# Performance work log

Hardware: AMD Instinct MI355X
Metric: run time of the kernel (lower is better)

Reference implementation:

```python
import jax, jax.numpy as jnp
import numpy as np

B, S, R, C_M = 1, 512, 256, 256   # batch, n_seq, n_res, msa channels
C_P, C_Z = 32, 128                # projection channels, pair channels


def setup_inputs() -> dict:
    key = jax.random.key(0)
    ks = jax.random.split(key, 8)
    M = jax.random.normal(ks[0], (B, S, R, C_M), dtype=jnp.float32)
    M_mask = jnp.ones((B, S, R), dtype=jnp.float32)
    Z_raw = jnp.zeros((B, R, R, C_Z), dtype=jnp.float32)
    # LayerNorm params
    ln_g = jnp.ones((C_M,), dtype=jnp.float32)
    ln_b = jnp.zeros((C_M,), dtype=jnp.float32)
    # linear_a / linear_b: glorot-uniform init
    lim = float(np.sqrt(6.0 / (C_M + C_P)))
    Wa = jax.random.uniform(ks[1], (C_P, C_M), minval=-lim, maxval=lim, dtype=jnp.float32)
    ba = jnp.zeros((C_P,), dtype=jnp.float32)
    Wb = jax.random.uniform(ks[2], (C_P, C_M), minval=-lim, maxval=lim, dtype=jnp.float32)
    bb = jnp.zeros((C_P,), dtype=jnp.float32)
    # o_linear is zero-initialized in the source; use small random weights so the
    # output is non-trivial for correctness testing (math is identical).
    Wo = jax.random.normal(ks[3], (C_Z, C_P * C_P), dtype=jnp.float32) * 0.02
    bo = jnp.zeros((C_Z,), dtype=jnp.float32)
    return {"M": M, "M_mask": M_mask, "Z_raw": Z_raw, "ln_g": ln_g, "ln_b": ln_b,
            "Wa": Wa, "ba": ba, "Wb": Wb, "bb": bb, "Wo": Wo, "bo": bo}


def _layernorm(x, g, b, eps=1e-5):
    mu = jnp.mean(x, axis=-1, keepdims=True)
    var = jnp.var(x, axis=-1, keepdims=True)
    return (x - mu) * jax.lax.rsqrt(var + eps) * g + b


def reference(M, M_mask, Z_raw, ln_g, ln_b, Wa, ba, Wb, bb, Wo, bo):
    Mn = _layernorm(M, ln_g, ln_b)                      # [b,s,i,c_m]
    mask = M_mask[..., None]                            # [b,s,i,1]
    left = (jnp.einsum('bsic,dc->bsid', Mn, Wa) + ba) * mask   # [b,s,i,d]
    right = (jnp.einsum('bsic,ec->bsie', Mn, Wb) + bb) * mask  # [b,s,j,e]
    # outer-product mean: contract over sequence dim s
    O = jnp.einsum('bsid,bsje->bijde', left, right)     # [b,i,j,d,e]
    b, i, j, d, e = O.shape
    O = O.reshape(b, i, j, d * e)
    Z = jnp.einsum('bijk,zk->bijz', O, Wo) + bo         # [b,i,j,c_z]
    norm = jnp.einsum('bsi,bsj->bij', M_mask, M_mask)[..., None]
    return Z / (1e-3 + norm)
```

## Files before the change

kernel.cpp:

```cpp
#include <hip/hip_runtime.h>
#include <hip/hip_bf16.h>
#include <stdint.h>

#define S_DIM 512
#define R_DIM 256
#define CM 256
#define CP 32
#define CZ 128

typedef __attribute__((ext_vector_type(8))) short bf16x8;
typedef __attribute__((ext_vector_type(4))) float f32x4;
typedef __attribute__((ext_vector_type(16))) float f32x16;
typedef unsigned int u32;

__device__ __forceinline__ float bf2f(unsigned short u) {
  union { u32 i; float f; } v; v.i = ((u32)u) << 16; return v.f;
}
__device__ __forceinline__ unsigned short f2bf(float f) {
  union { float f; u32 i; } v; v.f = f;
  u32 x = v.i;
  u32 r = (x + 0x7FFFu + ((x >> 16) & 1u)) >> 16;
  return (unsigned short)r;
}

__device__ __forceinline__ void gload_lds16(const unsigned short* g, unsigned short* l) {
  __builtin_amdgcn_global_load_lds((const __attribute__((address_space(1))) u32*)(g),
                                   (__attribute__((address_space(3))) u32*)(l), 16, 0, 0);
}

__device__ __forceinline__ void wave_bar() {
  asm volatile("" ::: "memory");
  __builtin_amdgcn_s_barrier();
  asm volatile("" ::: "memory");
}

__global__ __launch_bounds__(256) void
fused_prep_kernel(const float* __restrict__ Wa, const float* __restrict__ ba,
                  const float* __restrict__ Wb, const float* __restrict__ bb,
                  const float* __restrict__ ln_g, const float* __restrict__ ln_b,
                  const float* __restrict__ Wo, const float* __restrict__ mask,
                  unsigned short* __restrict__ wp, float* __restrict__ Ka,
                  float* __restrict__ Ca, unsigned short* __restrict__ Wo_bf,
                  float* __restrict__ scale) {
  const int b = blockIdx.x;
  const int t = threadIdx.x;
  if (b < 64) {
    __shared__ float ska[4], sca[4];
    const int o = b;
    const float* W = (o < 32) ? (Wa + o * CM) : (Wb + (o - 32) * CM);
    float wv = W[t];
    unsigned short bv = f2bf(wv * ln_g[t]);
    wp[o * CM + t] = bv;
    float ka = bf2f(bv);
    float ca = wv * ln_b[t];
    #pragma unroll
    for (int m = 1; m < 64; m <<= 1) {
      ka += __shfl_xor(ka, m);
      ca += __shfl_xor(ca, m);
    }
    if ((t & 63) == 0) { ska[t >> 6] = ka; sca[t >> 6] = ca; }
    __syncthreads();
    if (t == 0) {
      Ka[o] = ska[0] + ska[1] + ska[2] + ska[3];
      Ca[o] = sca[0] + sca[1] + sca[2] + sca[3] + ((o < 32) ? ba[o] : bb[o - 32]);
    }
  } else if (b < 576) {
    int idx = (b - 64) * 256 + t;
    int z = idx >> 10, k = idx & 1023;
    int d = k >> 5, e = k & 31;
    Wo_bf[(z << 10) + e * 32 + d] = f2bf(Wo[idx]);
  } else {
    const int i = b - 576, j = t;
    float sum = 0.f;
    for (int s = 0; s < S_DIM; ++s)
      sum += mask[s * R_DIM + i] * mask[s * R_DIM + j];
    scale[i * R_DIM + j] = 1.0f / (1e-3f + sum);
  }
}

#define K1_ROWS 64
#define XPAD 264

__global__ __launch_bounds__(256) void
ln_proj_kernel(const float* __restrict__ M, const float* __restrict__ mask,
               const unsigned short* __restrict__ wp_g, const float* __restrict__ Ka_g,
               const float* __restrict__ Ca_g,
               unsigned short* __restrict__ leftT, unsigned short* __restrict__ rightT) {
  __shared__ unsigned short xt[K1_ROWS * XPAD];
  __shared__ unsigned short wp[64 * XPAD];
  __shared__ float smu[K1_ROWS], srs[K1_ROWS], smk[K1_ROWS];
  __shared__ float sKa[64], sCa[64];

  const int t = threadIdx.x;
  const int lane = t & 63;
  const int w = t >> 6;
  const int lm = lane & 15;
  const int rr = lane >> 4;
  const int i = blockIdx.x;
  const int s0 = blockIdx.y * K1_ROWS;

  for (int idx = t; idx < 64 * CM / 8; idx += 256) {
    int row = idx >> 5;
    int col = (idx & 31) * 8;
    *(uint4*)(&wp[row * XPAD + col]) = *(const uint4*)(wp_g + row * CM + col);
  }
  if (t < 64) { sKa[t] = Ka_g[t]; sCa[t] = Ca_g[t]; }

  #pragma unroll
  for (int it = 0; it < 4; ++it) {
    const int row = w * 16 + it * 4 + rr;
    const int sg = s0 + row;
    const float* src = M + ((size_t)sg * R_DIM + i) * CM;
    float4 x[4];
    #pragma unroll
    for (int ch = 0; ch < 4; ++ch) x[ch] = *(const float4*)(src + ch * 64 + lm * 4);
    float sum = 0.f, ssq = 0.f;
    #pragma unroll
    for (int ch = 0; ch < 4; ++ch) {
      sum += x[ch].x + x[ch].y + x[ch].z + x[ch].w;
      ssq += x[ch].x * x[ch].x + x[ch].y * x[ch].y + x[ch].z * x[ch].z + x[ch].w * x[ch].w;
    }
    #pragma unroll
    for (int m = 1; m < 16; m <<= 1) {
      sum += __shfl_xor(sum, m);
      ssq += __shfl_xor(ssq, m);
    }
    float mu = sum * (1.0f / CM);
    float var = ssq * (1.0f / CM) - mu * mu;
    float rs = rsqrtf(var + 1e-5f);
    if (lm == 0) {
      smu[row] = mu; srs[row] = rs;
      smk[row] = mask[(size_t)sg * R_DIM + i];
    }
    #pragma unroll
    for (int ch = 0; ch < 4; ++ch) {
      ushort4 xb;
      xb.x = f2bf(x[ch].x); xb.y = f2bf(x[ch].y); xb.z = f2bf(x[ch].z); xb.w = f2bf(x[ch].w);
      *(ushort4*)(&xt[row * XPAD + ch * 64 + lm * 4]) = xb;
    }
  }
  __syncthreads();

  f32x4 acc[4] = {{0.f, 0.f, 0.f, 0.f}, {0.f, 0.f, 0.f, 0.f},
                  {0.f, 0.f, 0.f, 0.f}, {0.f, 0.f, 0.f, 0.f}};
  #pragma unroll
  for (int k = 0; k < 8; ++k) {
    const int c0 = k * 32 + ((lane >> 4) << 3);
    bf16x8 a = *(const bf16x8*)(&wp[(w * 16 + (lane & 15)) * XPAD + c0]);
    #pragma unroll
    for (int nt = 0; nt < 4; ++nt) {
      bf16x8 b = *(const bf16x8*)(&xt[(nt * 16 + (lane & 15)) * XPAD + c0]);
      acc[nt] = __builtin_amdgcn_mfma_f32_16x16x32_bf16(a, b, acc[nt], 0, 0, 0);
    }
  }

  #pragma unroll
  for (int nt = 0; nt < 4; ++nt) {
    int srow = nt * 16 + (lane & 15);
    float mu = smu[srow], rs = srs[srow], mk = smk[srow];
    int sg = s0 + srow;
    const size_t base = (size_t)(sg >> 3) * 65536 + (sg & 7);
    #pragma unroll
    for (int r = 0; r < 4; ++r) {
      int o = w * 16 + ((lane >> 4) << 2) + r;
      float v = (rs * (acc[nt][r] - mu * sKa[o]) + sCa[o]) * mk;
      unsigned short bv = f2bf(v);
      if (o < 32) leftT[base + (size_t)(i * 32 + o) * 8] = bv;
      else        rightT[base + (size_t)(i * 32 + (o - 32)) * 8] = bv;
    }
  }
}

#define NT2 8

__global__ __launch_bounds__(512, 1) void
opm_gemm_kernel(const unsigned short* __restrict__ leftT, const unsigned short* __restrict__ rightT,
                const unsigned short* __restrict__ Wo_bf, const float* __restrict__ bo,
                const float* __restrict__ scale, float* __restrict__ out) {
  extern __shared__ unsigned short smem[];

  const int t = threadIdx.x;
  const int lane = t & 63;
  const int l31 = lane & 31, lq2 = lane >> 5;
  const int w = t >> 6;
  const int wm = w >> 2, wn = w & 3;

  const int bid = blockIdx.x;
  const int xcd = bid & 7, local = bid >> 3;
  const int by = xcd * 4 + (local & 3);
  const int bx = local >> 2;

  const unsigned short* Asrc = leftT + (size_t)(by * 256) * 8;
  const unsigned short* Bsrc = rightT + (size_t)(bx * 256) * 8;

  int aoff[4], ldso[4];
  #pragma unroll
  for (int q = 0; q < 4; ++q) {
    int c = q * 512 + t;
    aoff[q] = (c >> 8) * 65536 + (c & 255) * 8;
    ldso[q] = c * 8;
  }

  f32x16 acc[4][2];
  #pragma unroll
  for (int a = 0; a < 4; ++a)
    #pragma unroll
    for (int b = 0; b < 2; ++b)
      #pragma unroll
      for (int r = 0; r < 16; ++r) acc[a][b][r] = 0.f;

  auto STAGE = [&](int kt, int buf) {
    const size_t kb = (size_t)kt * 8 * 65536;
    unsigned short* ab = smem + buf * 32768;
    #pragma unroll
    for (int q = 0; q < 4; ++q) {
      gload_lds16(Asrc + kb + aoff[q], ab + ldso[q]);
      gload_lds16(Bsrc + kb + aoff[q], ab + 16384 + ldso[q]);
    }
  };

  STAGE(0, 0);
  STAGE(1, 1);

  int arow[4], brow[2];
  #pragma unroll
  for (int mi = 0; mi < 4; ++mi) arow[mi] = (wm * 128 + mi * 32 + l31) * 8;
  #pragma unroll
  for (int ni = 0; ni < 2; ++ni) brow[ni] = 16384 + (wn * 64 + ni * 32 + l31) * 8;

  for (int kt = 0; kt < NT2; ++kt) {
    if (kt < NT2 - 1) asm volatile("s_waitcnt vmcnt(8)" ::: "memory");
    else              asm volatile("s_waitcnt vmcnt(0)" ::: "memory");
    wave_bar();

    const unsigned short* Ab = smem + (kt & 1) * 32768;
    #pragma unroll
    for (int ks = 0; ks < 4; ++ks) {
      const int kbase = (ks * 2 + lq2) * 2048;
      bf16x8 af[4], bf[2];
      #pragma unroll
      for (int mi = 0; mi < 4; ++mi) af[mi] = *(const bf16x8*)(Ab + kbase + arow[mi]);
      #pragma unroll
      for (int ni = 0; ni < 2; ++ni) bf[ni] = *(const bf16x8*)(Ab + kbase + brow[ni]);
      #pragma unroll
      for (int mi = 0; mi < 4; ++mi)
        #pragma unroll
        for (int ni = 0; ni < 2; ++ni)
          acc[mi][ni] = __builtin_amdgcn_mfma_f32_32x32x16_bf16(af[mi], bf[ni], acc[mi][ni], 0, 0, 0);
    }

    wave_bar();
    if (kt + 2 < NT2) STAGE(kt + 2, kt & 1);
  }

  #pragma unroll
  for (int mi = 0; mi < 4; ++mi) {
    #pragma unroll
    for (int ni = 0; ni < 2; ++ni) {
      const int pair = (wm * 4 + mi) * 8 + wn * 2 + ni;
      const u32 pbyte = (u32)((pair ^ l31) * 16 + lq2 * 8);
      #pragma unroll
      for (int g = 0; g < 4; ++g) {
        const u32 byte = (u32)(l31 * 4 + g) * 1024 + pbyte;
        ushort4 v4;
        v4.x = f2bf(acc[mi][ni][g * 4 + 0]);
        v4.y = f2bf(acc[mi][ni][g * 4 + 1]);
        v4.z = f2bf(acc[mi][ni][g * 4 + 2]);
        v4.w = f2bf(acc[mi][ni][g * 4 + 3]);
        *(ushort4*)((char*)smem + byte) = v4;
      }
    }
  }
  __syncthreads();

  f32x16 zacc;
  #pragma unroll
  for (int r = 0; r < 16; ++r) zacc[r] = 0.f;
  const unsigned short* wop = Wo_bf + (size_t)(wn * 32 + l31) * (CP * CP) + lq2 * 8;
  #pragma unroll 4
  for (int kk = 0; kk < 64; ++kk) {
    bf16x8 bw = *(const bf16x8*)(wop + kk * 16);
    const u32 ob = (u32)(kk * 2 + lq2) * 1024 + (u32)(((wm * 32 + l31) ^ (kk >> 1)) * 16);
    bf16x8 oa = *(const bf16x8*)((const char*)smem + ob);
    zacc = __builtin_amdgcn_mfma_f32_32x32x16_bf16(oa, bw, zacc, 0, 0, 0);
  }

  const int z = wn * 32 + l31;
  const float bz = bo[z];
  #pragma unroll
  for (int r = 0; r < 16; ++r) {
    const int pair = wm * 32 + (r & 3) + 8 * (r >> 2) + 4 * lq2;
    const int ig = by * 8 + (pair >> 3), jg = bx * 8 + (pair & 7);
    float v = (zacc[r] + bz) * scale[ig * R_DIM + jg];
    out[((size_t)ig * R_DIM + jg) * CZ + z] = v;
  }
}

extern "C" void kernel_launch(void* const* d_in, const int* in_sizes, int n_in,
                              void* d_out, int out_size, void* d_ws, size_t ws_size,
                              hipStream_t stream) {
  const float* M     = (const float*)d_in[0];
  const float* Mmask = (const float*)d_in[1];
  const float* ln_g  = (const float*)d_in[3];
  const float* ln_b  = (const float*)d_in[4];
  const float* Wa    = (const float*)d_in[5];
  const float* ba    = (const float*)d_in[6];
  const float* Wb    = (const float*)d_in[7];
  const float* bb    = (const float*)d_in[8];
  const float* Wo    = (const float*)d_in[9];
  const float* bo    = (const float*)d_in[10];
  float* out = (float*)d_out;

  char* ws = (char*)d_ws;
  unsigned short* leftT  = (unsigned short*)(ws);
  unsigned short* rightT = (unsigned short*)(ws + 8388608);
  unsigned short* wp     = (unsigned short*)(ws + 16777216);
  float*          Ka     = (float*)(ws + 16810240);
  float*          Ca     = (float*)(ws + 16810496);
  unsigned short* Wo_bf  = (unsigned short*)(ws + 16810752);
  float*          scale  = (float*)(ws + 17072896);
  (void)ws_size; (void)in_sizes; (void)n_in; (void)out_size;

  hipFuncSetAttribute((const void*)opm_gemm_kernel,
                      hipFuncAttributeMaxDynamicSharedMemorySize, 131072);

  hipLaunchKernelGGL(fused_prep_kernel, dim3(832), dim3(256), 0, stream,
                     Wa, ba, Wb, bb, ln_g, ln_b, Wo, Mmask, wp, Ka, Ca, Wo_bf, scale);
  hipLaunchKernelGGL(ln_proj_kernel, dim3(R_DIM, S_DIM / K1_ROWS), dim3(256), 0, stream,
                     M, Mmask, wp, Ka, Ca, leftT, rightT);
  hipLaunchKernelGGL(opm_gemm_kernel, dim3(1024), dim3(512), 131072, stream,
                     leftT, rightT, Wo_bf, bo, scale, out);
}
```

Before: 188.0 us.

## Vectorize projection stores, switch OPM GEMM to 16x16 MFMA, repack Wo layout

The projection kernel now stages its bf16 outputs in shared memory and writes them to leftT/rightT as 16-byte vector stores, replacing scattered 2-byte stores. The outer-product GEMM switches from 32x32x16 to 16x16x32 MFMA tiles with a new fragment mapping, a new swizzled LDS layout for the intermediate O tile, and Wo repacked so each kk step reads contiguous 8-element groups across z. The goal is to cut uncoalesced global writes and improve the memory access patterns of the second GEMM. In exchange it uses more LDS in the projection kernel, adds a block barrier there, and needs more accumulator registers in the GEMM.

```diff
diff --git a/kernel.cpp b/kernel.cpp
--- a/kernel.cpp
+++ b/kernel.cpp
@@ -68,7 +68,8 @@
     int idx = (b - 64) * 256 + t;
     int z = idx >> 10, k = idx & 1023;
     int d = k >> 5, e = k & 31;
-    Wo_bf[(z << 10) + e * 32 + d] = f2bf(Wo[idx]);
+    int kp = e * 32 + d;
+    Wo_bf[(kp >> 3) * 1024 + z * 8 + (kp & 7)] = f2bf(Wo[idx]);
   } else {
     const int i = b - 576, j = t;
     float sum = 0.f;
@@ -80,6 +81,7 @@
 
 #define K1_ROWS 64
 #define XPAD 264
+#define OTP 72
 
 __global__ __launch_bounds__(256) void
 ln_proj_kernel(const float* __restrict__ M, const float* __restrict__ mask,
@@ -88,6 +90,7 @@
                unsigned short* __restrict__ leftT, unsigned short* __restrict__ rightT) {
   __shared__ unsigned short xt[K1_ROWS * XPAD];
   __shared__ unsigned short wp[64 * XPAD];
+  __shared__ unsigned short ot[64 * OTP];
   __shared__ float smu[K1_ROWS], srs[K1_ROWS], smk[K1_ROWS];
   __shared__ float sKa[64], sCa[64];
 
@@ -158,16 +161,26 @@
   for (int nt = 0; nt < 4; ++nt) {
     int srow = nt * 16 + (lane & 15);
     float mu = smu[srow], rs = srs[srow], mk = smk[srow];
-    int sg = s0 + srow;
-    const size_t base = (size_t)(sg >> 3) * 65536 + (sg & 7);
     #pragma unroll
     for (int r = 0; r < 4; ++r) {
       int o = w * 16 + ((lane >> 4) << 2) + r;
       float v = (rs * (acc[nt][r] - mu * sKa[o]) + sCa[o]) * mk;
-      unsigned short bv = f2bf(v);
-      if (o < 32) leftT[base + (size_t)(i * 32 + o) * 8] = bv;
-      else        rightT[base + (size_t)(i * 32 + (o - 32)) * 8] = bv;
-    }
+      ot[o * OTP + srow] = f2bf(v);
+    }
+  }
+  __syncthreads();
+
+  #pragma unroll
+  for (int rep = 0; rep < 2; ++rep) {
+    int idx = rep * 256 + t;
+    int o = idx >> 3, sg = idx & 7;
+    ushort4 lo = *(const ushort4*)(&ot[o * OTP + sg * 8]);
+    ushort4 hi = *(const ushort4*)(&ot[o * OTP + sg * 8 + 4]);
+    size_t dst = (size_t)(blockIdx.y * 8 + sg) * 65536;
+    uint4 v; v.x = (u32)lo.x | ((u32)lo.y << 16); v.y = (u32)lo.z | ((u32)lo.w << 16);
+    v.z = (u32)hi.x | ((u32)hi.y << 16); v.w = (u32)hi.z | ((u32)hi.w << 16);
+    if (o < 32) *(uint4*)(leftT + dst + (size_t)(i * 32 + o) * 8) = v;
+    else        *(uint4*)(rightT + dst + (size_t)(i * 32 + (o - 32)) * 8) = v;
   }
 }
 
@@ -181,6 +194,7 @@
 
   const int t = threadIdx.x;
   const int lane = t & 63;
+  const int lm = lane & 15, lq = lane >> 4;
   const int l31 = lane & 31, lq2 = lane >> 5;
   const int w = t >> 6;
   const int wm = w >> 2, wn = w & 3;
@@ -193,41 +207,37 @@
   const unsigned short* Asrc = leftT + (size_t)(by * 256) * 8;
   const unsigned short* Bsrc = rightT + (size_t)(bx * 256) * 8;
 
-  int aoff[4], ldso[4];
+  int goff[4], ldso[4];
   #pragma unroll
   for (int q = 0; q < 4; ++q) {
     int c = q * 512 + t;
-    aoff[q] = (c >> 8) * 65536 + (c & 255) * 8;
+    goff[q] = (c >> 8) * 65536 + (c & 255) * 8;
     ldso[q] = c * 8;
   }
 
-  f32x16 acc[4][2];
-  #pragma unroll
-  for (int a = 0; a < 4; ++a)
-    #pragma unroll
-    for (int b = 0; b < 2; ++b)
-      #pragma unroll
-      for (int r = 0; r < 16; ++r) acc[a][b][r] = 0.f;
+  f32x4 acc[8][4];
+  #pragma unroll
+  for (int a = 0; a < 8; ++a)
+    #pragma unroll
+    for (int b = 0; b < 4; ++b) acc[a][b] = (f32x4){0.f, 0.f, 0.f, 0.f};
 
   auto STAGE = [&](int kt, int buf) {
     const size_t kb = (size_t)kt * 8 * 65536;
     unsigned short* ab = smem + buf * 32768;
     #pragma unroll
     for (int q = 0; q < 4; ++q) {
-      gload_lds16(Asrc + kb + aoff[q], ab + ldso[q]);
-      gload_lds16(Bsrc + kb + aoff[q], ab + 16384 + ldso[q]);
+      gload_lds16(Asrc + kb + goff[q], ab + ldso[q]);
+      gload_lds16(Bsrc + kb + goff[q], ab + 16384 + ldso[q]);
     }
   };
 
   STAGE(0, 0);
   STAGE(1, 1);
 
-  int arow[4], brow[2];
-  #pragma unroll
-  for (int mi = 0; mi < 4; ++mi) arow[mi] = (wm * 128 + mi * 32 + l31) * 8;
-  #pragma unroll
-  for (int ni = 0; ni < 2; ++ni) brow[ni] = 16384 + (wn * 64 + ni * 32 + l31) * 8;
-
+  const int abase = lq * 2048 + (wm * 128 + lm) * 8;
+  const int bbase = 16384 + lq * 2048 + (wn * 64 + lm) * 8;
+
+  #pragma unroll
   for (int kt = 0; kt < NT2; ++kt) {
     if (kt < NT2 - 1) asm volatile("s_waitcnt vmcnt(8)" ::: "memory");
     else              asm volatile("s_waitcnt vmcnt(0)" ::: "memory");
@@ -235,18 +245,19 @@
 
     const unsigned short* Ab = smem + (kt & 1) * 32768;
     #pragma unroll
-    for (int ks = 0; ks < 4; ++ks) {
-      const int kbase = (ks * 2 + lq2) * 2048;
-      bf16x8 af[4], bf[2];
+    for (int ks = 0; ks < 2; ++ks) {
+      bf16x8 af[8], bfr[4];
       #pragma unroll
-      for (int mi = 0; mi < 4; ++mi) af[mi] = *(const bf16x8*)(Ab + kbase + arow[mi]);
+      for (int mi = 0; mi < 8; ++mi)
+        af[mi] = *(const bf16x8*)(&Ab[abase + ks * 8192 + mi * 128]);
       #pragma unroll
-      for (int ni = 0; ni < 2; ++ni) bf[ni] = *(const bf16x8*)(Ab + kbase + brow[ni]);
+      for (int ni = 0; ni < 4; ++ni)
+        bfr[ni] = *(const bf16x8*)(&Ab[bbase + ks * 8192 + ni * 128]);
       #pragma unroll
-      for (int mi = 0; mi < 4; ++mi)
+      for (int mi = 0; mi < 8; ++mi)
         #pragma unroll
-        for (int ni = 0; ni < 2; ++ni)
-          acc[mi][ni] = __builtin_amdgcn_mfma_f32_32x32x16_bf16(af[mi], bf[ni], acc[mi][ni], 0, 0, 0);
+        for (int ni = 0; ni < 4; ++ni)
+          acc[mi][ni] = __builtin_amdgcn_mfma_f32_16x16x32_bf16(af[mi], bfr[ni], acc[mi][ni], 0, 0, 0);
     }
 
     wave_bar();
@@ -254,21 +265,20 @@
   }
 
   #pragma unroll
-  for (int mi = 0; mi < 4; ++mi) {
-    #pragma unroll
-    for (int ni = 0; ni < 2; ++ni) {
-      const int pair = (wm * 4 + mi) * 8 + wn * 2 + ni;
-      const u32 pbyte = (u32)((pair ^ l31) * 16 + lq2 * 8);
-      #pragma unroll
-      for (int g = 0; g < 4; ++g) {
-        const u32 byte = (u32)(l31 * 4 + g) * 1024 + pbyte;
-        ushort4 v4;
-        v4.x = f2bf(acc[mi][ni][g * 4 + 0]);
-        v4.y = f2bf(acc[mi][ni][g * 4 + 1]);
-        v4.z = f2bf(acc[mi][ni][g * 4 + 2]);
-        v4.w = f2bf(acc[mi][ni][g * 4 + 3]);
-        *(ushort4*)((char*)smem + byte) = v4;
-      }
+  for (int mi = 0; mi < 8; ++mi) {
+    const int m0 = wm * 128 + mi * 16 + lq * 4;
+    const int il = m0 >> 5, d0 = m0 & 31;
+    #pragma unroll
+    for (int ni = 0; ni < 4; ++ni) {
+      const int n = wn * 64 + ni * 16 + lm;
+      const int jl = n >> 5, e = n & 31;
+      const int pair = il * 8 + jl;
+      const int kg = e * 4 + (d0 >> 3);
+      const u32 byte = (u32)kg * 1024 + (u32)((pair ^ (kg >> 2) ^ (kg & 3)) * 16 + (d0 & 4) * 2);
+      ushort4 v4;
+      v4.x = f2bf(acc[mi][ni][0]); v4.y = f2bf(acc[mi][ni][1]);
+      v4.z = f2bf(acc[mi][ni][2]); v4.w = f2bf(acc[mi][ni][3]);
+      *(ushort4*)((char*)smem + byte) = v4;
     }
   }
   __syncthreads();
@@ -276,11 +286,12 @@
   f32x16 zacc;
   #pragma unroll
   for (int r = 0; r < 16; ++r) zacc[r] = 0.f;
-  const unsigned short* wop = Wo_bf + (size_t)(wn * 32 + l31) * (CP * CP) + lq2 * 8;
+  const unsigned short* wop = Wo_bf + lq2 * 1024 + (size_t)(wn * 32 + l31) * 8;
   #pragma unroll 4
   for (int kk = 0; kk < 64; ++kk) {
-    bf16x8 bw = *(const bf16x8*)(wop + kk * 16);
-    const u32 ob = (u32)(kk * 2 + lq2) * 1024 + (u32)(((wm * 32 + l31) ^ (kk >> 1)) * 16);
+    bf16x8 bw = *(const bf16x8*)(wop + kk * 2048);
+    const int kg = kk * 2 + lq2;
+    const u32 ob = (u32)kg * 1024 + (u32)((((wm * 32 + l31) ^ (kg >> 2) ^ (kg & 3))) * 16);
     bf16x8 oa = *(const bf16x8*)((const char*)smem + ob);
     zacc = __builtin_amdgcn_mfma_f32_32x32x16_bf16(oa, bw, zacc, 0, 0, 0);
   }
```

Result: faster. 166.8 us, median of 2 (-11.3%).
